# Performance work log

Hardware: AMD Instinct MI355X
Metric: run time of the kernel (lower is better)

Reference implementation:

```python
import jax, jax.numpy as jnp
import numpy as np
import math

N_EMBD = 1024
DIM_ATT = 1024
N_LAYER = 24
LAYER_ID = 12
B, T = 4, 4096


def _init_params():
    r01 = LAYER_ID / (N_LAYER - 1)
    r1a0 = 1.0 - LAYER_ID / N_LAYER
    ddd = np.arange(N_EMBD, dtype=np.float32) / N_EMBD
    h = np.arange(DIM_ATT, dtype=np.float32)
    decay_speed = -5.0 + 8.0 * (h / (DIM_ATT - 1)) ** (0.7 + 1.3 * r01)
    zigzag = (((np.arange(DIM_ATT) + 1) % 3) - 1).astype(np.float32) * 0.5
    time_first = np.float32(math.log(0.3)) + zigzag
    return {
        'time_decay': jnp.asarray(decay_speed, jnp.float32),
        'time_first': jnp.asarray(time_first, jnp.float32),
        'time_mix_k': jnp.asarray(ddd ** r1a0, jnp.float32),
        'time_mix_v': jnp.asarray(ddd ** r1a0 + 0.3 * r01, jnp.float32),
        'time_mix_r': jnp.asarray(ddd ** (0.5 * r1a0), jnp.float32),
    }


def setup_inputs() -> dict:
    key = jax.random.key(0)
    ks = jax.random.split(key, 5)
    inp = {'x': jax.random.normal(ks[0], (B, T, N_EMBD), jnp.float32)}
    inp.update(_init_params())
    s = 1.0 / math.sqrt(N_EMBD)
    inp['Wk'] = jax.random.normal(ks[1], (DIM_ATT, N_EMBD), jnp.float32) * s
    inp['Wv'] = jax.random.normal(ks[2], (DIM_ATT, N_EMBD), jnp.float32) * s
    inp['Wr'] = jax.random.normal(ks[3], (DIM_ATT, N_EMBD), jnp.float32) * s
    inp['Wo'] = jax.random.normal(ks[4], (N_EMBD, DIM_ATT), jnp.float32) * (1.0 / math.sqrt(DIM_ATT))
    return inp


def _wkv(w, u, k, v):
    # Numerically stable RWKV-4 WKV recurrence. w = -exp(time_decay) <= 0.
    # k, v: [B, T, C]; w, u: [C]. Scan over T with [B, C] state.
    def step(carry, kv):
        aa, bb, pp = carry
        kt, vt = kv
        ww = u + kt
        p = jnp.maximum(pp, ww)
        e1 = jnp.exp(pp - p)
        e2 = jnp.exp(ww - p)
        y = (e1 * aa + e2 * vt) / (e1 * bb + e2)
        ww2 = pp + w
        p2 = jnp.maximum(ww2, kt)
        e1b = jnp.exp(ww2 - p2)
        e2b = jnp.exp(kt - p2)
        return (e1b * aa + e2b * vt, e1b * bb + e2b, p2), y

    Bb, Tt, C = k.shape
    init = (jnp.zeros((Bb, C), k.dtype), jnp.zeros((Bb, C), k.dtype),
            jnp.full((Bb, C), -1e38, k.dtype))
    _, ys = jax.lax.scan(step, init, (jnp.swapaxes(k, 0, 1), jnp.swapaxes(v, 0, 1)))
    return jnp.swapaxes(ys, 0, 1)


def reference(x, time_decay, time_first, time_mix_k, time_mix_v, time_mix_r, Wk, Wv, Wr, Wo):
    # time_shift: ZeroPad2d((0,0,1,-1)) -> shift right by 1 along T with zero fill
    xx = jnp.pad(x, ((0, 0), (1, 0), (0, 0)))[:, :-1]
    xk = x * time_mix_k + xx * (1.0 - time_mix_k)
    xv = x * time_mix_v + xx * (1.0 - time_mix_v)
    xr = x * time_mix_r + xx * (1.0 - time_mix_r)
    k = jnp.einsum('btc,dc->btd', xk, Wk)
    v = jnp.einsum('btc,dc->btd', xv, Wv)
    sr = jax.nn.sigmoid(jnp.einsum('btc,dc->btd', xr, Wr))
    w = -jnp.exp(time_decay)  # as in the WKV CUDA kernel
    rwkv = sr * _wkv(w, time_first, k, v)
    return jnp.einsum('btd,cd->btc', rwkv, Wo)
```

## Files before the change

kernel.cpp:

```cpp
#include <hip/hip_runtime.h>
#include <hip/hip_bf16.h>
#include <stdint.h>

#define B_ 4
#define T_ 4096
#define C_ 1024
#define D_ 1024
#define NC_ 64
#define LC_ 64

typedef __bf16 bf16x8 __attribute__((ext_vector_type(8)));
typedef float  f32x4  __attribute__((ext_vector_type(4)));

__device__ __forceinline__ unsigned short f2bf(float f) {
    union { float f; unsigned u; } c; c.f = f;
    return (unsigned short)((c.u + 0x7fffu + ((c.u >> 16) & 1u)) >> 16);
}

__global__ void cast_bf16_kernel(const float* __restrict__ s, unsigned short* __restrict__ d) {
    int i = blockIdx.x * blockDim.x + threadIdx.x;
    float4 v = *reinterpret_cast<const float4*>(s + ((size_t)i << 2));
    ushort4 o;
    o.x = f2bf(v.x); o.y = f2bf(v.y); o.z = f2bf(v.z); o.w = f2bf(v.w);
    *reinterpret_cast<ushort4*>(d + ((size_t)i << 2)) = o;
}

__global__ void mix_cast_kernel(const float* __restrict__ x,
                                const float* __restrict__ mk,
                                const float* __restrict__ mv,
                                const float* __restrict__ mr,
                                unsigned short* __restrict__ xk,
                                unsigned short* __restrict__ xv,
                                unsigned short* __restrict__ xr) {
    int i = blockIdx.x * blockDim.x + threadIdx.x;
    int base = i << 2;
    int c = base & (C_ - 1);
    int m = base >> 10;
    int t = m & (T_ - 1);
    float4 xc = *reinterpret_cast<const float4*>(x + base);
    float4 xp = make_float4(0.f, 0.f, 0.f, 0.f);
    if (t != 0) xp = *reinterpret_cast<const float4*>(x + base - C_);
    float4 k4 = *reinterpret_cast<const float4*>(mk + c);
    float4 v4 = *reinterpret_cast<const float4*>(mv + c);
    float4 r4 = *reinterpret_cast<const float4*>(mr + c);
    ushort4 ok, ov, orr;
    ok.x  = f2bf(xp.x + k4.x * (xc.x - xp.x));
    ok.y  = f2bf(xp.y + k4.y * (xc.y - xp.y));
    ok.z  = f2bf(xp.z + k4.z * (xc.z - xp.z));
    ok.w  = f2bf(xp.w + k4.w * (xc.w - xp.w));
    ov.x  = f2bf(xp.x + v4.x * (xc.x - xp.x));
    ov.y  = f2bf(xp.y + v4.y * (xc.y - xp.y));
    ov.z  = f2bf(xp.z + v4.z * (xc.z - xp.z));
    ov.w  = f2bf(xp.w + v4.w * (xc.w - xp.w));
    orr.x = f2bf(xp.x + r4.x * (xc.x - xp.x));
    orr.y = f2bf(xp.y + r4.y * (xc.y - xp.y));
    orr.z = f2bf(xp.z + r4.z * (xc.z - xp.z));
    orr.w = f2bf(xp.w + r4.w * (xc.w - xp.w));
    *reinterpret_cast<ushort4*>(xk + base) = ok;
    *reinterpret_cast<ushort4*>(xv + base) = ov;
    *reinterpret_cast<ushort4*>(xr + base) = orr;
}

template<bool SIG>
__global__ __launch_bounds__(256) void gemm_bt(const unsigned short* __restrict__ A,
                                               const unsigned short* __restrict__ Bw,
                                               float* __restrict__ Cm) {
    __shared__ __align__(16) unsigned short As[128 * 32];
    __shared__ __align__(16) unsigned short Bs[128 * 32];
    const int tid  = threadIdx.x;
    const int lane = tid & 63;
    const int wid  = tid >> 6;
    const int bn = (blockIdx.x & 7) << 7;
    const int bm = (blockIdx.x >> 3) << 7;
    const int wr = (wid >> 1) * 64;
    const int wc = (wid & 1) * 64;

    f32x4 acc[4][4] = {};

    const int r0 = tid >> 2;
    const int ck = (tid & 3) * 8;
    const unsigned short* ga = A  + (size_t)(bm + r0) * 1024 + ck;
    const unsigned short* gb = Bw + (size_t)(bn + r0) * 1024 + ck;

    uint4 ra0 = *reinterpret_cast<const uint4*>(ga);
    uint4 ra1 = *reinterpret_cast<const uint4*>(ga + 64 * 1024);
    uint4 rb0 = *reinterpret_cast<const uint4*>(gb);
    uint4 rb1 = *reinterpret_cast<const uint4*>(gb + 64 * 1024);

    const int arow = wr + (lane & 15);
    const int brow = wc + (lane & 15);
    const int ko   = (lane >> 4) * 8;
    const int wofs = r0 * 32 + ck;

    for (int ks = 0; ks < 32; ++ks) {
        __syncthreads();
        *reinterpret_cast<uint4*>(&As[wofs])        = ra0;
        *reinterpret_cast<uint4*>(&As[wofs + 2048]) = ra1;
        *reinterpret_cast<uint4*>(&Bs[wofs])        = rb0;
        *reinterpret_cast<uint4*>(&Bs[wofs + 2048]) = rb1;
        __syncthreads();
        if (ks < 31) {
            ga += 32; gb += 32;
            ra0 = *reinterpret_cast<const uint4*>(ga);
            ra1 = *reinterpret_cast<const uint4*>(ga + 64 * 1024);
            rb0 = *reinterpret_cast<const uint4*>(gb);
            rb1 = *reinterpret_cast<const uint4*>(gb + 64 * 1024);
        }
        bf16x8 af[4], bfr[4];
        #pragma unroll
        for (int i = 0; i < 4; ++i) {
            af[i]  = *reinterpret_cast<const bf16x8*>(&As[(arow + i * 16) * 32 + ko]);
            bfr[i] = *reinterpret_cast<const bf16x8*>(&Bs[(brow + i * 16) * 32 + ko]);
        }
        #pragma unroll
        for (int i = 0; i < 4; ++i)
            #pragma unroll
            for (int j = 0; j < 4; ++j)
                acc[i][j] = __builtin_amdgcn_mfma_f32_16x16x32_bf16(af[i], bfr[j], acc[i][j], 0, 0, 0);
    }

    const int row0 = bm + wr + (lane >> 4) * 4;
    const int col0 = bn + wc + (lane & 15);
    #pragma unroll
    for (int i = 0; i < 4; ++i)
        #pragma unroll
        for (int j = 0; j < 4; ++j)
            #pragma unroll
            for (int r = 0; r < 4; ++r) {
                float vv = acc[i][j][r];
                if (SIG) vv = 1.0f / (1.0f + __expf(-vv));
                Cm[(size_t)(row0 + i * 16 + r) * 1024 + col0 + j * 16] = vv;
            }
}

__global__ void wkv_chunk(const float* __restrict__ k, const float* __restrict__ v,
                          const float* __restrict__ td,
                          float* __restrict__ ca, float* __restrict__ cb, float* __restrict__ cp,
                          int NB) {
    int gid = blockIdx.x * 256 + threadIdx.x;
    int d   = gid & (D_ - 1);
    int rem = gid >> 10;
    int j   = rem & (NC_ - 1);
    int b   = rem >> 6;
    float w = -__expf(td[d]);
    size_t base = ((size_t)(b * T_ + j * LC_)) * D_ + d;
    float aa = 0.f, bb = 0.f, pp = -1e38f;
    for (int t = 0; t < LC_; ++t) {
        float kt = k[base + (size_t)t * D_];
        float vt = v[base + (size_t)t * D_];
        float ww = pp + w;
        float p  = fmaxf(ww, kt);
        float e1 = __expf(ww - p);
        float e2 = __expf(kt - p);
        aa = e1 * aa + e2 * vt;
        bb = e1 * bb + e2;
        pp = p;
    }
    int ch  = (b << 10) + d;
    int idx = j * (NB << 10) + ch;
    ca[idx] = aa;
    cb[idx] = bb;
    cp[idx] = pp;
}

__global__ void wkv_scan(const float* __restrict__ ca, const float* __restrict__ cb,
                         const float* __restrict__ cp, const float* __restrict__ td,
                         float* __restrict__ sa, float* __restrict__ sb, float* __restrict__ sp,
                         int NB) {
    int ch = blockIdx.x * 256 + threadIdx.x;
    int d  = ch & (D_ - 1);
    float w  = -__expf(td[d]);
    float wL = w * (float)LC_;
    float A = 0.f, Bv = 0.f, P = -1e38f;
    int stride = NB << 10;
    for (int j = 0; j < NC_; ++j) {
        int idx = j * stride + ch;
        sa[idx] = A; sb[idx] = Bv; sp[idx] = P;
        float a2 = ca[idx], b2 = cb[idx], p2 = cp[idx];
        float Pd = P + wL;
        float pm = fmaxf(Pd, p2);
        float e1 = __expf(Pd - pm);
        float e2 = __expf(p2 - pm);
        A  = e1 * A  + e2 * a2;
        Bv = e1 * Bv + e2 * b2;
        P  = pm;
    }
}

__global__ void wkv_emit(const float* __restrict__ k, const float* __restrict__ v,
                         const float* __restrict__ sr, const float* __restrict__ td,
                         const float* __restrict__ tf,
                         const float* __restrict__ sa, const float* __restrict__ sb,
                         const float* __restrict__ sp,
                         unsigned short* __restrict__ ybf, int NB) {
    int gid = blockIdx.x * 256 + threadIdx.x;
    int d   = gid & (D_ - 1);
    int rem = gid >> 10;
    int j   = rem & (NC_ - 1);
    int b   = rem >> 6;
    int ch  = (b << 10) + d;
    float w = -__expf(td[d]);
    float u = tf[d];
    int idx = j * (NB << 10) + ch;
    float aa = sa[idx], bb = sb[idx], pp = sp[idx];
    size_t base = ((size_t)(b * T_ + j * LC_)) * D_ + d;
    for (int t = 0; t < LC_; ++t) {
        size_t o = base + (size_t)t * D_;
        float kt = k[o];
        float vt = v[o];
        float ww = u + kt;
        float p  = fmaxf(pp, ww);
        float e1 = __expf(pp - p);
        float e2 = __expf(ww - p);
        float y  = (e1 * aa + e2 * vt) / (e1 * bb + e2);
        ybf[o] = f2bf(sr[o] * y);
        float ww2 = pp + w;
        float p2  = fmaxf(ww2, kt);
        float e1b = __expf(ww2 - p2);
        float e2b = __expf(kt - p2);
        aa = e1b * aa + e2b * vt;
        bb = e1b * bb + e2b;
        pp = p2;
    }
}

extern "C" void kernel_launch(void* const* d_in, const int* in_sizes, int n_in,
                              void* d_out, int out_size, void* d_ws, size_t ws_size,
                              hipStream_t stream) {
    const float* x  = (const float*)d_in[0];
    const float* td = (const float*)d_in[1];
    const float* tf = (const float*)d_in[2];
    const float* mk = (const float*)d_in[3];
    const float* mv = (const float*)d_in[4];
    const float* mr = (const float*)d_in[5];
    const float* Wk = (const float*)d_in[6];
    const float* Wv = (const float*)d_in[7];
    const float* Wr = (const float*)d_in[8];
    const float* Wo = (const float*)d_in[9];
    float* out = (float*)d_out;

    char* ws = (char*)d_ws;
    unsigned short* wkbf = (unsigned short*)(ws + ((size_t)0 << 20));
    unsigned short* wvbf = (unsigned short*)(ws + ((size_t)2 << 20));
    unsigned short* wrbf = (unsigned short*)(ws + ((size_t)4 << 20));
    unsigned short* wobf = (unsigned short*)(ws + ((size_t)6 << 20));

    cast_bf16_kernel<<<1024, 256, 0, stream>>>(Wk, wkbf);
    cast_bf16_kernel<<<1024, 256, 0, stream>>>(Wv, wvbf);
    cast_bf16_kernel<<<1024, 256, 0, stream>>>(Wr, wrbf);
    cast_bf16_kernel<<<1024, 256, 0, stream>>>(Wo, wobf);

    if (ws_size >= ((size_t)240 << 20)) {
        unsigned short* xk = (unsigned short*)(ws + ((size_t)8  << 20));
        unsigned short* xv = (unsigned short*)(ws + ((size_t)40 << 20));
        unsigned short* xr = (unsigned short*)(ws + ((size_t)72 << 20));
        float* kb  = (float*)(ws + ((size_t)104 << 20));
        float* vb  = (float*)(ws + ((size_t)168 << 20));
        float* srb = (float*)(ws + ((size_t)8   << 20));
        unsigned short* ybf = xr;
        float* ca = (float*)(ws + ((size_t)232 << 20));
        float* cb = ca + (1u << 18);
        float* cp = cb + (1u << 18);
        float* sa = cp + (1u << 18);
        float* sb = sa + (1u << 18);
        float* sp = sb + (1u << 18);

        mix_cast_kernel<<<16384, 256, 0, stream>>>(x, mk, mv, mr, xk, xv, xr);
        gemm_bt<false><<<1024, 256, 0, stream>>>(xk, wkbf, kb);
        gemm_bt<false><<<1024, 256, 0, stream>>>(xv, wvbf, vb);
        gemm_bt<true ><<<1024, 256, 0, stream>>>(xr, wrbf, srb);
        wkv_chunk<<<1024, 256, 0, stream>>>(kb, vb, td, ca, cb, cp, 4);
        wkv_scan<<<16, 256, 0, stream>>>(ca, cb, cp, td, sa, sb, sp, 4);
        wkv_emit<<<1024, 256, 0, stream>>>(kb, vb, srb, td, tf, sa, sb, sp, ybf, 4);
        gemm_bt<false><<<1024, 256, 0, stream>>>(ybf, wobf, out);
    } else {
        unsigned short* xk = (unsigned short*)(ws + ((size_t)8  << 20));
        unsigned short* xv = (unsigned short*)(ws + ((size_t)16 << 20));
        unsigned short* xr = (unsigned short*)(ws + ((size_t)24 << 20));
        float* kb  = (float*)(ws + ((size_t)32 << 20));
        float* vb  = (float*)(ws + ((size_t)48 << 20));
        float* srb = (float*)(ws + ((size_t)64 << 20));
        float* ca  = (float*)(ws + ((size_t)80 << 20));
        float* cb  = ca + (1u << 16);
        float* cp  = cb + (1u << 16);
        float* sa  = cp + (1u << 16);
        float* sb  = sa + (1u << 16);
        float* sp  = sb + (1u << 16);
        unsigned short* ybf = xk;

        for (int b = 0; b < B_; ++b) {
            const float* xb = x + (size_t)b * T_ * C_;
            float* outb = out + (size_t)b * T_ * C_;
            mix_cast_kernel<<<4096, 256, 0, stream>>>(xb, mk, mv, mr, xk, xv, xr);
            gemm_bt<false><<<256, 256, 0, stream>>>(xk, wkbf, kb);
            gemm_bt<false><<<256, 256, 0, stream>>>(xv, wvbf, vb);
            gemm_bt<true ><<<256, 256, 0, stream>>>(xr, wrbf, srb);
            wkv_chunk<<<256, 256, 0, stream>>>(kb, vb, td, ca, cb, cp, 1);
            wkv_scan<<<4, 256, 0, stream>>>(ca, cb, cp, td, sa, sb, sp, 1);
            wkv_emit<<<256, 256, 0, stream>>>(kb, vb, srb, td, tf, sa, sb, sp, ybf, 1);
            gemm_bt<false><<<256, 256, 0, stream>>>(ybf, wobf, outb);
        }
    }
}
```

Baseline: 478.4 us.

## Load GEMM tiles directly to LDS and remap blocks per XCD

The GEMM now stages A and B tiles with global_load_lds, which writes straight into shared memory and skips the register round-trip. The block index is also remapped so that each XCD handles a contiguous band of M-tiles across all N-tiles, which is meant to improve L2 reuse of A. The cost is that the register prefetch is gone: each iteration now issues its loads and then waits on vmcnt(0) before any MFMA work, so load latency is no longer hidden behind compute. The LDS layout must match the per-wave contiguous writes of the builtin.

Measured after the change: 472.5 us. Within noise of the previous version (-1.2%).

```diff
diff --git a/kernel.cpp b/kernel.cpp
--- a/kernel.cpp
+++ b/kernel.cpp
@@ -15,6 +15,13 @@
 __device__ __forceinline__ unsigned short f2bf(float f) {
     union { float f; unsigned u; } c; c.f = f;
     return (unsigned short)((c.u + 0x7fffu + ((c.u >> 16) & 1u)) >> 16);
+}
+
+__device__ __forceinline__ void gload_lds16(const unsigned short* g, unsigned short* l) {
+    __builtin_amdgcn_global_load_lds(
+        (const __attribute__((address_space(1))) void*)g,
+        (__attribute__((address_space(3))) void*)l,
+        16, 0, 0);
 }
 
 __global__ void cast_bf16_kernel(const float* __restrict__ s, unsigned short* __restrict__ d) {
@@ -70,8 +77,10 @@
     const int tid  = threadIdx.x;
     const int lane = tid & 63;
     const int wid  = tid >> 6;
-    const int bn = (blockIdx.x & 7) << 7;
-    const int bm = (blockIdx.x >> 3) << 7;
+    const int xcd   = blockIdx.x & 7;
+    const int local = blockIdx.x >> 3;
+    const int bm = (((xcd << 4) + (local >> 3))) << 7;
+    const int bn = (local & 7) << 7;
     const int wr = (wid >> 1) * 64;
     const int wc = (wid & 1) * 64;
 
@@ -79,33 +88,29 @@
 
     const int r0 = tid >> 2;
     const int ck = (tid & 3) * 8;
-    const unsigned short* ga = A  + (size_t)(bm + r0) * 1024 + ck;
-    const unsigned short* gb = Bw + (size_t)(bn + r0) * 1024 + ck;
-
-    uint4 ra0 = *reinterpret_cast<const uint4*>(ga);
-    uint4 ra1 = *reinterpret_cast<const uint4*>(ga + 64 * 1024);
-    uint4 rb0 = *reinterpret_cast<const uint4*>(gb);
-    uint4 rb1 = *reinterpret_cast<const uint4*>(gb + 64 * 1024);
+    const unsigned short* ga0 = A  + (size_t)(bm + r0) * 1024 + ck;
+    const unsigned short* gb0 = Bw + (size_t)(bn + r0) * 1024 + ck;
+    const unsigned short* ga1 = ga0 + (size_t)64 * 1024;
+    const unsigned short* gb1 = gb0 + (size_t)64 * 1024;
+    unsigned short* lA0 = As + wid * 512;
+    unsigned short* lA1 = As + 2048 + wid * 512;
+    unsigned short* lB0 = Bs + wid * 512;
+    unsigned short* lB1 = Bs + 2048 + wid * 512;
 
     const int arow = wr + (lane & 15);
     const int brow = wc + (lane & 15);
     const int ko   = (lane >> 4) * 8;
-    const int wofs = r0 * 32 + ck;
 
     for (int ks = 0; ks < 32; ++ks) {
         __syncthreads();
-        *reinterpret_cast<uint4*>(&As[wofs])        = ra0;
-        *reinterpret_cast<uint4*>(&As[wofs + 2048]) = ra1;
-        *reinterpret_cast<uint4*>(&Bs[wofs])        = rb0;
-        *reinterpret_cast<uint4*>(&Bs[wofs + 2048]) = rb1;
+        gload_lds16(ga0, lA0);
+        gload_lds16(ga1, lA1);
+        gload_lds16(gb0, lB0);
+        gload_lds16(gb1, lB1);
+        ga0 += 32; ga1 += 32; gb0 += 32; gb1 += 32;
+        asm volatile("s_waitcnt vmcnt(0)" ::: "memory");
         __syncthreads();
-        if (ks < 31) {
-            ga += 32; gb += 32;
-            ra0 = *reinterpret_cast<const uint4*>(ga);
-            ra1 = *reinterpret_cast<const uint4*>(ga + 64 * 1024);
-            rb0 = *reinterpret_cast<const uint4*>(gb);
-            rb1 = *reinterpret_cast<const uint4*>(gb + 64 * 1024);
-        }
+
         bf16x8 af[4], bfr[4];
         #pragma unroll
         for (int i = 0; i < 4; ++i) {
```
